# Performance work log

Measured on AMD Instinct MI355X. Metric: run time of the kernel, lower is better.

## Reference

```python
import jax, jax.numpy as jnp
import numpy as np


def _unpack_int4(packed, in_features):
    # packed: [out, in/2] with uint8 semantics (values in [0, 256)).
    low = packed & 15           # even columns
    high = (packed >> 4) & 15   # odd columns
    out_f = packed.shape[0]
    doubled = jnp.stack([low, high], axis=-1).reshape(out_f, packed.shape[1] * 2)
    doubled = jnp.where(doubled >= 8, doubled - 16, doubled)  # sign-extend int4
    return doubled[:, :in_features].astype(jnp.int8)


def setup_inputs() -> dict:
    key = jax.random.key(0)
    k1, k2, k3, k4 = jax.random.split(key, 4)
    B, S, IN, OUT = 8, 512, 4096, 11008
    x = jax.random.normal(k1, (B, S, IN), dtype=jnp.float32)
    weight_packed = jax.random.randint(k2, (OUT, IN // 2), 0, 256, dtype=jnp.int32)
    scale = jax.random.uniform(k3, (OUT, 1), dtype=jnp.float32) * 0.01 + 1e-4
    bias = jax.random.normal(k4, (OUT,), dtype=jnp.float32)
    return {"x": x, "weight_packed": weight_packed, "scale": scale, "bias": bias}


def reference(x, weight_packed, scale, bias):
    in_features = weight_packed.shape[1] * 2
    w_int = _unpack_int4(weight_packed, in_features)          # [out, in] int8
    w_deq = w_int.astype(x.dtype) * scale.astype(x.dtype)     # [out, in]
    # F.linear: x @ W^T + b
    return jnp.einsum('bsi,oi->bso', x, w_deq) + bias.astype(x.dtype)
```

## Files before the change

kernel.cpp:

```cpp
#include <hip/hip_runtime.h>

typedef __attribute__((ext_vector_type(8))) short bf16x8;
typedef __attribute__((ext_vector_type(4))) float f32x4;
typedef __attribute__((ext_vector_type(8))) unsigned short u16x8;

#define MDIM 4096
#define NDIM 11008
#define KDIM 4096
#define KP   (KDIM / 2)

__device__ __forceinline__ unsigned short f2bf(float f) {
  unsigned int u = __float_as_uint(f);
  u += 0x7FFFu + ((u >> 16) & 1u);
  return (unsigned short)(u >> 16);
}


__global__ __launch_bounds__(256) void cvt_x_kernel(const float* __restrict__ X,
                                                    unsigned short* __restrict__ Xb) {
  const int stride = gridDim.x * blockDim.x;
  for (int i = blockIdx.x * blockDim.x + threadIdx.x; i < (MDIM * KDIM / 8); i += stride) {
    const float4 f0 = ((const float4*)X)[2 * i];
    const float4 f1 = ((const float4*)X)[2 * i + 1];
    ushort4 a, b;
    a.x = f2bf(f0.x); a.y = f2bf(f0.y); a.z = f2bf(f0.z); a.w = f2bf(f0.w);
    b.x = f2bf(f1.x); b.y = f2bf(f1.y); b.z = f2bf(f1.z); b.w = f2bf(f1.w);
    ((ushort4*)Xb)[2 * i]     = a;
    ((ushort4*)Xb)[2 * i + 1] = b;
  }
}

__global__ __launch_bounds__(256) void unpack_w_kernel(const int* __restrict__ Wp,
                                                       unsigned short* __restrict__ Wb) {
  const int stride = gridDim.x * blockDim.x;
  const int n4 = NDIM * KP / 4;
  for (int i = blockIdx.x * blockDim.x + threadIdx.x; i < n4; i += stride) {
    const int4 v = ((const int4*)Wp)[i];
    const int vv[4] = {v.x, v.y, v.z, v.w};
    u16x8 s;
    #pragma unroll
    for (int j = 0; j < 4; ++j) {
      const int lo = ((vv[j] & 15) ^ 8) - 8;
      const int hi = (((vv[j] >> 4) & 15) ^ 8) - 8;
      s[2 * j]     = f2bf((float)lo);
      s[2 * j + 1] = f2bf((float)hi);
    }
    *(u16x8*)(Wb + 8 * (size_t)i) = s;
  }
}


#define GNWG ((MDIM / 128) * (NDIM / 128))

__global__ __launch_bounds__(256, 2)
void gemm_bf16_kernel(const unsigned short* __restrict__ Xb,
                      const unsigned short* __restrict__ Wb,
                      const float* __restrict__ scale,
                      const float* __restrict__ bias,
                      float* __restrict__ Out) {
  __shared__ alignas(16) unsigned short As[2][128 * 32];
  __shared__ alignas(16) unsigned short Bs[2][128 * 32];

  const int t    = threadIdx.x;
  const int lane = t & 63;
  const int wid  = t >> 6;
  const int wm   = wid >> 1;
  const int wn   = wid & 1;
  const int lr   = lane & 15;
  const int kg   = lane >> 4;

  const int wg  = (blockIdx.x & 7) * (GNWG >> 3) + (blockIdx.x >> 3);
  const int bm  = wg & 31;
  const int bn  = wg >> 5;
  const int row0 = bm * 128;
  const int col0 = bn * 128;

  auto stage = [&](int kt, int buf) {
    #pragma unroll
    for (int j = 0; j < 2; ++j) {
      const int s  = j * 256 + t;
      const int r  = s >> 2;
      const int ks = s & 3;
      const unsigned short* ga = Xb + (size_t)(row0 + r) * KDIM + kt * 32 + ks * 8;
      const unsigned short* gb = Wb + (size_t)(col0 + r) * KDIM + kt * 32 + ks * 8;
      unsigned short* la = &As[buf][(j * 256 + wid * 64) * 8];
      unsigned short* lb = &Bs[buf][(j * 256 + wid * 64) * 8];
      __builtin_amdgcn_global_load_lds(
          (const __attribute__((address_space(1))) unsigned int*)ga,
          (__attribute__((address_space(3))) unsigned int*)la, 16, 0, 0);
      __builtin_amdgcn_global_load_lds(
          (const __attribute__((address_space(1))) unsigned int*)gb,
          (__attribute__((address_space(3))) unsigned int*)lb, 16, 0, 0);
    }
  };

  f32x4 acc[4][4];
  #pragma unroll
  for (int i = 0; i < 4; ++i)
    #pragma unroll
    for (int j = 0; j < 4; ++j)
      #pragma unroll
      for (int e = 0; e < 4; ++e)
        acc[i][j][e] = 0.0f;

  auto compute = [&](int buf) {
    bf16x8 a[4], b[4];
    #pragma unroll
    for (int mi = 0; mi < 4; ++mi)
      a[mi] = *(const bf16x8*)&As[buf][(wm * 64 + mi * 16 + lr) * 32 + kg * 8];
    #pragma unroll
    for (int ni = 0; ni < 4; ++ni)
      b[ni] = *(const bf16x8*)&Bs[buf][(wn * 64 + ni * 16 + lr) * 32 + kg * 8];
    #pragma unroll
    for (int mi = 0; mi < 4; ++mi)
      #pragma unroll
      for (int ni = 0; ni < 4; ++ni)
        acc[mi][ni] = __builtin_amdgcn_mfma_f32_16x16x32_bf16(
            a[mi], b[ni], acc[mi][ni], 0, 0, 0);
  };

  stage(0, 0);
  __syncthreads();

  for (int kt = 0; kt < KDIM / 32; kt += 2) {
    if (kt + 1 < KDIM / 32) stage(kt + 1, 1);
    compute(0);
    __syncthreads();
    if (kt + 2 < KDIM / 32) stage(kt + 2, 0);
    compute(1);
    __syncthreads();
  }

  #pragma unroll
  for (int ni = 0; ni < 4; ++ni) {
    const int n = col0 + wn * 64 + ni * 16 + lr;
    const float sc = scale[n];
    const float bz = bias[n];
    #pragma unroll
    for (int mi = 0; mi < 4; ++mi) {
      const int m0 = row0 + wm * 64 + mi * 16 + (kg << 2);
      #pragma unroll
      for (int j = 0; j < 4; ++j)
        Out[(size_t)(m0 + j) * NDIM + n] = acc[mi][ni][j] * sc + bz;
    }
  }
}


__global__ __launch_bounds__(256, 2)
void int4_linear_fused_kernel(const float* __restrict__ X,
                              const int* __restrict__ Wp,
                              const float* __restrict__ scale,
                              const float* __restrict__ bias,
                              float* __restrict__ Out)
{
  __shared__ alignas(16) unsigned short As[2][128][40];
  __shared__ alignas(16) unsigned short Bs[2][128][40];

  const int t    = threadIdx.x;
  const int lane = t & 63;
  const int wid  = t >> 6;
  const int wm   = wid >> 1;
  const int wn   = wid & 1;
  const int lr   = lane & 15;
  const int kg   = lane >> 4;

  const int NWG = GNWG;
  const int wg  = (blockIdx.x & 7) * (NWG >> 3) + (blockIdx.x >> 3);
  const int bm  = wg & 31;
  const int bn  = wg >> 5;
  const int row0 = bm * 128;
  const int col0 = bn * 128;

  const int arow = t >> 3;
  const int acol = (t & 7) << 2;
  const int brow  = t >> 1;
  const int bhalf = t & 1;

  const float* Abase = X  + (size_t)(row0 + arow) * KDIM + acol;
  const int*   Bbase = Wp + (size_t)(col0 + brow) * KP + (bhalf << 3);

  float4 aR[4];
  int4   bR[2];

  f32x4 acc[4][4];
  #pragma unroll
  for (int i = 0; i < 4; ++i)
    #pragma unroll
    for (int j = 0; j < 4; ++j)
      #pragma unroll
      for (int e = 0; e < 4; ++e)
        acc[i][j][e] = 0.0f;

  auto loadG = [&](int kt) {
    const float* ap = Abase + kt * 32;
    #pragma unroll
    for (int p = 0; p < 4; ++p)
      aR[p] = *(const float4*)(ap + (size_t)p * 32 * KDIM);
    const int* bp = Bbase + kt * 16;
    bR[0] = *(const int4*)bp;
    bR[1] = *(const int4*)(bp + 4);
  };

  auto stageL = [&](int buf) {
    #pragma unroll
    for (int p = 0; p < 4; ++p) {
      ushort4 u;
      u.x = f2bf(aR[p].x);
      u.y = f2bf(aR[p].y);
      u.z = f2bf(aR[p].z);
      u.w = f2bf(aR[p].w);
      *(ushort4*)&As[buf][arow + p * 32][acol] = u;
    }
    #pragma unroll
    for (int q = 0; q < 2; ++q) {
      const int vv[4] = {q ? bR[1].x : bR[0].x, q ? bR[1].y : bR[0].y,
                         q ? bR[1].z : bR[0].z, q ? bR[1].w : bR[0].w};
      u16x8 s;
      #pragma unroll
      for (int j = 0; j < 4; ++j) {
        const int lo = ((vv[j] & 15) ^ 8) - 8;
        const int hi = (((vv[j] >> 4) & 15) ^ 8) - 8;
        s[2 * j]     = f2bf((float)lo);
        s[2 * j + 1] = f2bf((float)hi);
      }
      *(u16x8*)&Bs[buf][brow][(bhalf << 4) + (q << 3)] = s;
    }
  };

  auto compute = [&](int buf) {
    bf16x8 a[4], b[4];
    #pragma unroll
    for (int mi = 0; mi < 4; ++mi)
      a[mi] = *(const bf16x8*)&As[buf][wm * 64 + mi * 16 + lr][kg * 8];
    #pragma unroll
    for (int ni = 0; ni < 4; ++ni)
      b[ni] = *(const bf16x8*)&Bs[buf][wn * 64 + ni * 16 + lr][kg * 8];
    #pragma unroll
    for (int mi = 0; mi < 4; ++mi)
      #pragma unroll
      for (int ni = 0; ni < 4; ++ni)
        acc[mi][ni] = __builtin_amdgcn_mfma_f32_16x16x32_bf16(
            a[mi], b[ni], acc[mi][ni], 0, 0, 0);
  };

  loadG(0);
  stageL(0);
  __syncthreads();

  for (int kt = 0; kt < KDIM / 32; ++kt) {
    const int cur = kt & 1;
    if (kt + 1 < KDIM / 32) loadG(kt + 1);
    compute(cur);
    if (kt + 1 < KDIM / 32) stageL(cur ^ 1);
    __syncthreads();
  }

  #pragma unroll
  for (int ni = 0; ni < 4; ++ni) {
    const int n = col0 + wn * 64 + ni * 16 + lr;
    const float sc = scale[n];
    const float bz = bias[n];
    #pragma unroll
    for (int mi = 0; mi < 4; ++mi) {
      const int m0 = row0 + wm * 64 + mi * 16 + (kg << 2);
      #pragma unroll
      for (int j = 0; j < 4; ++j)
        Out[(size_t)(m0 + j) * NDIM + n] = acc[mi][ni][j] * sc + bz;
    }
  }
}


extern "C" void kernel_launch(void* const* d_in, const int* in_sizes, int n_in,
                              void* d_out, int out_size, void* d_ws, size_t ws_size,
                              hipStream_t stream) {
  const float* x     = (const float*)d_in[0];
  const int*   wp    = (const int*)d_in[1];
  const float* scale = (const float*)d_in[2];
  const float* bias  = (const float*)d_in[3];
  float* out = (float*)d_out;

  const size_t need = ((size_t)MDIM * KDIM + (size_t)NDIM * KDIM) * 2;

  if (ws_size >= need) {
    unsigned short* Xb = (unsigned short*)d_ws;
    unsigned short* Wb = Xb + (size_t)MDIM * KDIM;
    hipLaunchKernelGGL(cvt_x_kernel,    dim3(2048), dim3(256), 0, stream, x, Xb);
    hipLaunchKernelGGL(unpack_w_kernel, dim3(2048), dim3(256), 0, stream, wp, Wb);
    hipLaunchKernelGGL(gemm_bf16_kernel, dim3(GNWG), dim3(256), 0, stream,
                       Xb, Wb, scale, bias, out);
  } else {
    hipLaunchKernelGGL(int4_linear_fused_kernel, dim3(GNWG), dim3(256), 0, stream,
                       x, wp, scale, bias, out);
  }
}
```

Baseline: 760.3 us.

## Add 256x128 bf16 GEMM with triple-buffered direct-to-LDS loads and swizzle

Replaces the 128x128 bf16 GEMM stage with a 256x128 tile kernel using 512 threads, K-step 64, and a three-stage LDS ring filled by global_load_lds with an XOR swizzle to avoid bank conflicts. The larger tile raises arithmetic intensity per workgroup, and the deeper pipeline with vmcnt-based waits overlaps loads with MFMA. It uses 144KB of dynamic LDS at one workgroup per CU and falls back to the old kernel if the attribute call fails.

```diff
diff --git a/kernel.cpp b/kernel.cpp
--- a/kernel.cpp
+++ b/kernel.cpp
@@ -46,6 +46,136 @@
       s[2 * j + 1] = f2bf((float)hi);
     }
     *(u16x8*)(Wb + 8 * (size_t)i) = s;
+  }
+}
+
+
+#define BM2 256
+#define BN2 128
+#define NT2 (KDIM / 64)
+#define NWG2 ((MDIM / BM2) * (NDIM / BN2))
+#define BUFSZ 24576
+#define LDSB  (3 * BUFSZ * 2)
+
+__global__ __launch_bounds__(512, 1)
+void gemm_bf16_256_kernel(const unsigned short* __restrict__ Xb,
+                          const unsigned short* __restrict__ Wb,
+                          const float* __restrict__ scale,
+                          const float* __restrict__ bias,
+                          float* __restrict__ Out) {
+  extern __shared__ unsigned short lds[];
+
+  const int t    = threadIdx.x;
+  const int lane = t & 63;
+  const int wid  = t >> 6;
+  const int wr   = wid >> 1;
+  const int wc   = wid & 1;
+  const int lr   = lane & 15;
+  const int kg   = lane >> 4;
+
+  const int wg   = (blockIdx.x & 7) * (NWG2 >> 3) + (blockIdx.x >> 3);
+  const int bm   = wg & 15;
+  const int bn   = wg >> 4;
+  const int row0 = bm * BM2;
+  const int col0 = bn * BN2;
+
+  auto stage = [&](int kt, int buf) {
+    unsigned short* Ab = lds + buf * BUFSZ;
+    unsigned short* Bb = Ab + 16384;
+    #pragma unroll
+    for (int p = 0; p < 4; ++p) {
+      const int s  = p * 512 + t;
+      const int r  = s >> 3;
+      const int ks = (s & 7) ^ (r & 7);
+      const unsigned short* ga = Xb + (size_t)(row0 + r) * KDIM + kt * 64 + ks * 8;
+      unsigned short* la = Ab + (p * 512 + wid * 64) * 8;
+      __builtin_amdgcn_global_load_lds(
+          (const __attribute__((address_space(1))) unsigned int*)ga,
+          (__attribute__((address_space(3))) unsigned int*)la, 16, 0, 0);
+    }
+    #pragma unroll
+    for (int p = 0; p < 2; ++p) {
+      const int s  = p * 512 + t;
+      const int r  = s >> 3;
+      const int ks = (s & 7) ^ (r & 7);
+      const unsigned short* gb = Wb + (size_t)(col0 + r) * KDIM + kt * 64 + ks * 8;
+      unsigned short* lb = Bb + (p * 512 + wid * 64) * 8;
+      __builtin_amdgcn_global_load_lds(
+          (const __attribute__((address_space(1))) unsigned int*)gb,
+          (__attribute__((address_space(3))) unsigned int*)lb, 16, 0, 0);
+    }
+  };
+
+  f32x4 acc[4][4];
+  #pragma unroll
+  for (int i = 0; i < 4; ++i)
+    #pragma unroll
+    for (int j = 0; j < 4; ++j)
+      #pragma unroll
+      for (int e = 0; e < 4; ++e)
+        acc[i][j][e] = 0.0f;
+
+  auto compute = [&](int buf) {
+    const unsigned short* Ab = lds + buf * BUFSZ;
+    const unsigned short* Bb = Ab + 16384;
+    #pragma unroll
+    for (int ks = 0; ks < 2; ++ks) {
+      bf16x8 a[4], b[4];
+      #pragma unroll
+      for (int mi = 0; mi < 4; ++mi) {
+        const int r  = wr * 64 + mi * 16 + lr;
+        const int sl = (ks * 4 + kg) ^ (r & 7);
+        a[mi] = *(const bf16x8*)&Ab[r * 64 + sl * 8];
+      }
+      #pragma unroll
+      for (int ni = 0; ni < 4; ++ni) {
+        const int r  = wc * 64 + ni * 16 + lr;
+        const int sl = (ks * 4 + kg) ^ (r & 7);
+        b[ni] = *(const bf16x8*)&Bb[r * 64 + sl * 8];
+      }
+      #pragma unroll
+      for (int mi = 0; mi < 4; ++mi)
+        #pragma unroll
+        for (int ni = 0; ni < 4; ++ni)
+          acc[mi][ni] = __builtin_amdgcn_mfma_f32_16x16x32_bf16(
+              a[mi], b[ni], acc[mi][ni], 0, 0, 0);
+    }
+  };
+
+  stage(0, 0);
+  stage(1, 1);
+  asm volatile("s_waitcnt vmcnt(6)" ::: "memory");
+  __builtin_amdgcn_s_barrier();
+
+  int buf = 0;
+  for (int kt = 0; kt < NT2; ++kt) {
+    if (kt + 2 < NT2) {
+      int b2 = buf + 2; if (b2 >= 3) b2 -= 3;
+      stage(kt + 2, b2);
+    }
+    compute(buf);
+    if (kt == NT2 - 1) break;
+    if (kt + 2 < NT2) {
+      asm volatile("s_waitcnt vmcnt(6)" ::: "memory");
+    } else {
+      asm volatile("s_waitcnt vmcnt(0)" ::: "memory");
+    }
+    __builtin_amdgcn_s_barrier();
+    ++buf; if (buf == 3) buf = 0;
+  }
+
+  #pragma unroll
+  for (int ni = 0; ni < 4; ++ni) {
+    const int n = col0 + wc * 64 + ni * 16 + lr;
+    const float sc = scale[n];
+    const float bz = bias[n];
+    #pragma unroll
+    for (int mi = 0; mi < 4; ++mi) {
+      const int m0 = row0 + wr * 64 + mi * 16 + (kg << 2);
+      #pragma unroll
+      for (int j = 0; j < 4; ++j)
+        Out[(size_t)(m0 + j) * NDIM + n] = acc[mi][ni][j] * sc + bz;
+    }
   }
 }
 
@@ -165,8 +295,7 @@
   const int lr   = lane & 15;
   const int kg   = lane >> 4;
 
-  const int NWG = GNWG;
-  const int wg  = (blockIdx.x & 7) * (NWG >> 3) + (blockIdx.x >> 3);
+  const int wg  = (blockIdx.x & 7) * (GNWG >> 3) + (blockIdx.x >> 3);
   const int bm  = wg & 31;
   const int bn  = wg >> 5;
   const int row0 = bm * 128;
@@ -288,8 +417,17 @@
     unsigned short* Wb = Xb + (size_t)MDIM * KDIM;
     hipLaunchKernelGGL(cvt_x_kernel,    dim3(2048), dim3(256), 0, stream, x, Xb);
     hipLaunchKernelGGL(unpack_w_kernel, dim3(2048), dim3(256), 0, stream, wp, Wb);
-    hipLaunchKernelGGL(gemm_bf16_kernel, dim3(GNWG), dim3(256), 0, stream,
-                       Xb, Wb, scale, bias, out);
+
+    hipError_t attr_ok = hipFuncSetAttribute(
+        (const void*)gemm_bf16_256_kernel,
+        hipFuncAttributeMaxDynamicSharedMemorySize, LDSB);
+    if (attr_ok == hipSuccess) {
+      hipLaunchKernelGGL(gemm_bf16_256_kernel, dim3(NWG2), dim3(512), LDSB, stream,
+                         Xb, Wb, scale, bias, out);
+    } else {
+      hipLaunchKernelGGL(gemm_bf16_kernel, dim3(GNWG), dim3(256), 0, stream,
+                         Xb, Wb, scale, bias, out);
+    }
   } else {
     hipLaunchKernelGGL(int4_linear_fused_kernel, dim3(GNWG), dim3(256), 0, stream,
                        x, wp, scale, bias, out);
```

After: 687.5 us. 1.11x faster.
